# Kernel optimization log

Measured on AMD Instinct MI355X. Metric: run time of the kernel, lower is better.

Reference implementation:

```python
import jax, jax.numpy as jnp
import numpy as np

DIM = 2048
NHEAD = 16
HEAD_DIM = DIM // NHEAD
FF_HIDDEN = 5632
EPS = 1e-6


def setup_inputs() -> dict:
    key = jax.random.key(0)
    ks = jax.random.split(key, 8)
    B, S = 2, 2048
    sd = 0.02
    return {
        "x": jax.random.normal(ks[0], (B, S, DIM), dtype=jnp.float32),
        "w_qkv": jax.random.normal(ks[1], (DIM, 3 * DIM), dtype=jnp.float32) * sd,
        "w_out": jax.random.normal(ks[2], (DIM, DIM), dtype=jnp.float32) * sd,
        "g1": jnp.ones((DIM,), dtype=jnp.float32),
        "g2": jnp.ones((DIM,), dtype=jnp.float32),
        "w1": jax.random.normal(ks[3], (DIM, FF_HIDDEN), dtype=jnp.float32) * sd,
        "w3": jax.random.normal(ks[4], (DIM, FF_HIDDEN), dtype=jnp.float32) * sd,
        "w2": jax.random.normal(ks[5], (FF_HIDDEN, DIM), dtype=jnp.float32) * sd,
    }


def _rmsnorm(x, g):
    rms = jnp.sqrt(jnp.mean(x * x, axis=-1, keepdims=True) + EPS)
    return x / rms * g


def _attention(x, w_qkv, w_out):
    B, S, D = x.shape
    qkv = x @ w_qkv  # [B,S,3D]
    q, k, v = jnp.split(qkv, 3, axis=-1)
    # [B,H,S,hd]
    q = q.reshape(B, S, NHEAD, HEAD_DIM).transpose(0, 2, 1, 3)
    k = k.reshape(B, S, NHEAD, HEAD_DIM).transpose(0, 2, 1, 3)
    v = v.reshape(B, S, NHEAD, HEAD_DIM).transpose(0, 2, 1, 3)
    scores = jnp.einsum("bhqd,bhkd->bhqk", q, k) / jnp.sqrt(jnp.float32(HEAD_DIM))
    causal = jnp.tril(jnp.ones((S, S), dtype=bool))
    scores = jnp.where(causal, scores, -jnp.inf)
    attn = jax.nn.softmax(scores, axis=-1)
    out = jnp.einsum("bhqk,bhkd->bhqd", attn, v)
    out = out.transpose(0, 2, 1, 3).reshape(B, S, D)
    return out @ w_out


def _swiglu(x, w1, w3, w2):
    return (jax.nn.silu(x @ w1) * (x @ w3)) @ w2


def reference(x, w_qkv, w_out, g1, g2, w1, w3, w2):
    x = x + _attention(_rmsnorm(x, g1), w_qkv, w_out)
    x = x + _swiglu(_rmsnorm(x, g2), w1, w3, w2)
    return x
```

## Files before the change

### kernel.cpp

```cpp
#include <hip/hip_runtime.h>
#include <hip/hip_bf16.h>
#include <stdint.h>


typedef __attribute__((ext_vector_type(8))) short bf16x8;
typedef __attribute__((ext_vector_type(8))) unsigned short u16x8;
typedef __attribute__((ext_vector_type(4))) float f32x4;

__device__ __forceinline__ unsigned short f2bf(float f) {
  union { float f; unsigned int u; } c; c.f = f;
  unsigned int u = c.u + 0x7fffu + ((c.u >> 16) & 1u);
  return (unsigned short)(u >> 16);
}
__device__ __forceinline__ float bf2f(unsigned short h) {
  union { unsigned int u; float f; } c; c.u = ((unsigned int)h) << 16;
  return c.f;
}

__device__ __forceinline__ void gload16(const void* g, void* l) {
  __builtin_amdgcn_global_load_lds(
      (const __attribute__((address_space(1))) void*)g,
      (__attribute__((address_space(3))) void*)l, 16, 0, 0);
}

__global__ __launch_bounds__(256)
void rmsnorm_bf16(const float* __restrict__ x, const float* __restrict__ g,
                  unsigned short* __restrict__ y)
{
  const long row = blockIdx.x;
  const float* xr = x + row * 2048;
  const int t = threadIdx.x;
  float4 a = *(const float4*)(xr + t * 8);
  float4 b = *(const float4*)(xr + t * 8 + 4);
  float ss = a.x*a.x + a.y*a.y + a.z*a.z + a.w*a.w
           + b.x*b.x + b.y*b.y + b.z*b.z + b.w*b.w;
#pragma unroll
  for (int off = 32; off >= 1; off >>= 1) ss += __shfl_xor(ss, off, 64);
  __shared__ float sm[4];
  if ((t & 63) == 0) sm[t >> 6] = ss;
  __syncthreads();
  float inv = rsqrtf((sm[0] + sm[1] + sm[2] + sm[3]) * (1.0f / 2048.0f) + 1e-6f);
  float4 ga = *(const float4*)(g + t * 8);
  float4 gb = *(const float4*)(g + t * 8 + 4);
  u16x8 ov;
  ov[0] = f2bf(a.x * inv * ga.x); ov[1] = f2bf(a.y * inv * ga.y);
  ov[2] = f2bf(a.z * inv * ga.z); ov[3] = f2bf(a.w * inv * ga.w);
  ov[4] = f2bf(b.x * inv * gb.x); ov[5] = f2bf(b.y * inv * gb.y);
  ov[6] = f2bf(b.z * inv * gb.z); ov[7] = f2bf(b.w * inv * gb.w);
  *(u16x8*)(y + row * 2048 + t * 8) = ov;
}

__global__ __launch_bounds__(256)
void transpose_w(const float* __restrict__ in, unsigned short* __restrict__ outp,
                 int K, int N)
{
  __shared__ float tile[32][33];
  const int c0 = blockIdx.x * 32, r0 = blockIdx.y * 32;
  const int cx = threadIdx.x & 31, ry = threadIdx.x >> 5;
#pragma unroll
  for (int i = 0; i < 4; i++)
    tile[ry + i * 8][cx] = in[(long)(r0 + ry + i * 8) * N + c0 + cx];
  __syncthreads();
#pragma unroll
  for (int i = 0; i < 4; i++)
    outp[(long)(c0 + ry + i * 8) * K + r0 + cx] = f2bf(tile[cx][ry + i * 8]);
}

template<int EPI>
__global__ __launch_bounds__(256)
void gemm_bt(const unsigned short* __restrict__ A,
             const unsigned short* __restrict__ Bt,
             void* __restrict__ Cout,
             const float* __restrict__ res,
             const unsigned short* __restrict__ mulsrc,
             int M, int N, int K)
{
  __shared__ unsigned short lds[2 * 128 * 64];
  const int tid = threadIdx.x;
  const int lane = tid & 63, wave = tid >> 6;
  const int wr = wave >> 1, wc = wave & 1;
  const int l15 = lane & 15, lg = lane >> 4;
  const long m0 = (long)blockIdx.y * 128, n0 = (long)blockIdx.x * 128;

  f32x4 acc[4][4];
#pragma unroll
  for (int m = 0; m < 4; m++)
#pragma unroll
    for (int n = 0; n < 4; n++) acc[m][n] = f32x4{0.f, 0.f, 0.f, 0.f};

  const int rsub = lane >> 3;
  const int csw  = (lane & 7) ^ rsub;
  const unsigned short* Ab = A  + (m0 + wave * 32 + rsub) * (long)K + csw * 8;
  const unsigned short* Bb = Bt + (n0 + wave * 32 + rsub) * (long)K + csw * 8;
  unsigned short* Al = lds + wave * 2048;
  unsigned short* Bl = lds + 8192 + wave * 2048;

  for (int kt = 0; kt < K; kt += 64) {
    __syncthreads();
#pragma unroll
    for (int i = 0; i < 4; i++) {
      gload16(Ab + (long)(i * 8) * K + kt, Al + i * 512);
      gload16(Bb + (long)(i * 8) * K + kt, Bl + i * 512);
    }
    __syncthreads();
#pragma unroll
    for (int kc = 0; kc < 2; kc++) {
      bf16x8 af[4], bfr[4];
#pragma unroll
      for (int m = 0; m < 4; m++) {
        int row = wr * 64 + m * 16 + l15;
        int off = row * 128 + ((kc * 64 + lg * 16) ^ ((row & 7) << 4));
        af[m] = *(const bf16x8*)((const char*)lds + off);
      }
#pragma unroll
      for (int n = 0; n < 4; n++) {
        int row = wc * 64 + n * 16 + l15;
        int off = 16384 + row * 128 + ((kc * 64 + lg * 16) ^ ((row & 7) << 4));
        bfr[n] = *(const bf16x8*)((const char*)lds + off);
      }
#pragma unroll
      for (int m = 0; m < 4; m++)
#pragma unroll
        for (int n = 0; n < 4; n++)
          acc[m][n] = __builtin_amdgcn_mfma_f32_16x16x32_bf16(af[m], bfr[n], acc[m][n], 0, 0, 0);
    }
  }

  if (EPI == 3) {
#pragma unroll
    for (int m = 0; m < 4; m++)
#pragma unroll
      for (int n = 0; n < 4; n++)
#pragma unroll
        for (int r = 0; r < 4; r++) {
          long row = m0 + wr * 64 + m * 16 + lg * 4 + r;
          long col = n0 + wc * 64 + n * 16 + l15;
          ((float*)Cout)[row * N + col] = acc[m][n][r] + res[row * N + col];
        }
    return;
  }

  __syncthreads();
  unsigned short* Cl = lds;
#pragma unroll
  for (int m = 0; m < 4; m++)
#pragma unroll
    for (int n = 0; n < 4; n++)
#pragma unroll
      for (int r = 0; r < 4; r++) {
        float v = acc[m][n][r];
        if (EPI == 1) v = v / (1.f + __expf(-v));
        Cl[(wr * 64 + m * 16 + lg * 4 + r) * 128 + wc * 64 + n * 16 + l15] = f2bf(v);
      }
  __syncthreads();
#pragma unroll
  for (int r8 = 0; r8 < 8; r8++) {
    int id = tid + r8 * 256;
    int row = id >> 4, c = (id & 15) * 8;
    long grow = m0 + row, gcol = n0 + c;
    u16x8 v = *(const u16x8*)(Cl + row * 128 + c);
    if (EPI == 2) {
      u16x8 mm = *(const u16x8*)(mulsrc + grow * N + gcol);
#pragma unroll
      for (int j = 0; j < 8; j++) v[j] = f2bf(bf2f(v[j]) * bf2f(mm[j]));
    }
    *(u16x8*)((unsigned short*)Cout + grow * N + gcol) = v;
  }
}

__global__ __launch_bounds__(256)
void attn_fwd(const unsigned short* __restrict__ qkv, unsigned short* __restrict__ out)
{
  __shared__ unsigned short Klds[64 * 128];
  __shared__ unsigned short Vt[128 * 64];
  __shared__ unsigned short Plds[4][16 * 64];
  const int tid = threadIdx.x, lane = tid & 63, w = tid >> 6;
  const int l15 = lane & 15, lg = lane >> 4;
  const int qb = blockIdx.x * 64;
  const int b = blockIdx.y >> 4, hh = blockIdx.y & 15;
  const long rstride = 6144;
  const long base = (long)b * 2048 * 6144;
  const int qoff = hh * 128, koff = 2048 + hh * 128, voff = 4096 + hh * 128;

  bf16x8 qf[4];
  {
    long qrow = qb + w * 16 + l15;
#pragma unroll
    for (int kc = 0; kc < 4; kc++)
      qf[kc] = *(const bf16x8*)(qkv + base + qrow * rstride + qoff + kc * 32 + lg * 8);
  }
  f32x4 o[8];
#pragma unroll
  for (int dg = 0; dg < 8; dg++) o[dg] = f32x4{0.f, 0.f, 0.f, 0.f};
  float mrow[4] = {-1e30f, -1e30f, -1e30f, -1e30f};
  float lrow[4] = {0.f, 0.f, 0.f, 0.f};
  const float scale = 0.08838834764831845f;

  const int s_st = tid >> 4;
  const int d0 = (tid & 15) * 8;

  const int nt = blockIdx.x + 1;
  for (int t = 0; t < nt; t++) {
    const long kvb = base + (long)(t * 64) * rstride;
#pragma unroll
    for (int i = 0; i < 4; i++) {
      int srow = s_st + i * 16;
      uint4 kk = *(const uint4*)(qkv + kvb + (long)srow * rstride + koff + d0);
      *(uint4*)((char*)Klds + ((srow * 256 + d0 * 2) ^ ((srow & 7) << 4))) = kk;
      u16x8 vv = *(const u16x8*)(qkv + kvb + (long)srow * rstride + voff + d0);
#pragma unroll
      for (int j = 0; j < 8; j++) {
        int d = d0 + j;
        int xr = (((d >> 3) ^ d) & 7) << 4;
        *((unsigned short*)((char*)Vt + ((d * 128 + srow * 2) ^ xr))) = vv[j];
      }
    }
    __syncthreads();

    f32x4 sacc[4];
#pragma unroll
    for (int cg = 0; cg < 4; cg++) {
      f32x4 a = f32x4{0.f, 0.f, 0.f, 0.f};
#pragma unroll
      for (int kc = 0; kc < 4; kc++) {
        int krow = cg * 16 + l15;
        bf16x8 kf = *(const bf16x8*)((char*)Klds +
                      ((krow * 256 + kc * 64 + lg * 16) ^ ((krow & 7) << 4)));
        a = __builtin_amdgcn_mfma_f32_16x16x32_bf16(qf[kc], kf, a, 0, 0, 0);
      }
      sacc[cg] = a;
    }

    float p[4][4];
    float pm[4];
    const bool diag = (t == nt - 1);
#pragma unroll
    for (int r = 0; r < 4; r++) pm[r] = -1e30f;
#pragma unroll
    for (int cg = 0; cg < 4; cg++)
#pragma unroll
      for (int r = 0; r < 4; r++) {
        float v = sacc[cg][r] * scale;
        if (diag) {
          int kvg = t * 64 + cg * 16 + l15;
          int qg = qb + w * 16 + lg * 4 + r;
          if (kvg > qg) v = -1e30f;
        }
        p[cg][r] = v;
        pm[r] = fmaxf(pm[r], v);
      }
#pragma unroll
    for (int r = 0; r < 4; r++) {
#pragma unroll
      for (int off = 1; off < 16; off <<= 1)
        pm[r] = fmaxf(pm[r], __shfl_xor(pm[r], off, 64));
      float mn = fmaxf(mrow[r], pm[r]);
      float al = __expf(mrow[r] - mn);
      mrow[r] = mn;
      float s = 0.f;
#pragma unroll
      for (int cg = 0; cg < 4; cg++) { p[cg][r] = __expf(p[cg][r] - mn); s += p[cg][r]; }
#pragma unroll
      for (int off = 1; off < 16; off <<= 1)
        s += __shfl_xor(s, off, 64);
      lrow[r] = lrow[r] * al + s;
#pragma unroll
      for (int dg = 0; dg < 8; dg++) o[dg][r] *= al;
    }

#pragma unroll
    for (int cg = 0; cg < 4; cg++)
#pragma unroll
      for (int r = 0; r < 4; r++) {
        int q = lg * 4 + r;
        *((unsigned short*)((char*)&Plds[w][0] +
            ((q * 128 + (cg * 16 + l15) * 2) ^ ((q & 7) << 4)))) = f2bf(p[cg][r]);
      }
    asm volatile("s_waitcnt lgkmcnt(0)" ::: "memory");
    __builtin_amdgcn_sched_barrier(0);

#pragma unroll
    for (int kc = 0; kc < 2; kc++) {
      bf16x8 pa = *(const bf16x8*)((char*)&Plds[w][0] +
                    ((l15 * 128 + kc * 64 + lg * 16) ^ ((l15 & 7) << 4)));
#pragma unroll
      for (int dg = 0; dg < 8; dg++) {
        int d = dg * 16 + l15;
        int xr = (((d >> 3) ^ d) & 7) << 4;
        bf16x8 vf = *(const bf16x8*)((char*)Vt + ((d * 128 + kc * 64 + lg * 16) ^ xr));
        o[dg] = __builtin_amdgcn_mfma_f32_16x16x32_bf16(pa, vf, o[dg], 0, 0, 0);
      }
    }
    __syncthreads();
  }

#pragma unroll
  for (int r = 0; r < 4; r++) {
    float inv = 1.f / lrow[r];
    long row = (long)b * 2048 + qb + w * 16 + lg * 4 + r;
#pragma unroll
    for (int dg = 0; dg < 8; dg++)
      out[row * 2048 + hh * 128 + dg * 16 + l15] = f2bf(o[dg][r] * inv);
  }
}

extern "C" void kernel_launch(void* const* d_in, const int* in_sizes, int n_in,
                              void* d_out, int out_size, void* d_ws, size_t ws_size,
                              hipStream_t stream)
{
  const float* x     = (const float*)d_in[0];
  const float* w_qkv = (const float*)d_in[1];
  const float* w_out = (const float*)d_in[2];
  const float* g1    = (const float*)d_in[3];
  const float* g2    = (const float*)d_in[4];
  const float* w1    = (const float*)d_in[5];
  const float* w3    = (const float*)d_in[6];
  const float* w2    = (const float*)d_in[7];
  float* outp = (float*)d_out;
  char* ws = (char*)d_ws;

  unsigned short* wT  = (unsigned short*)(ws);
  unsigned short* y   = (unsigned short*)(ws + 25165824);
  unsigned short* qkv = (unsigned short*)(ws + 41943040);
  unsigned short* att = (unsigned short*)(ws + 92274688);
  float*          x1  = (float*)(ws + 109051904);
  unsigned short* s1  = (unsigned short*)(ws + 142606336);
  unsigned short* h   = qkv;

  rmsnorm_bf16<<<4096, 256, 0, stream>>>(x, g1, y);
  transpose_w<<<dim3(6144 / 32, 2048 / 32), 256, 0, stream>>>(w_qkv, wT, 2048, 6144);
  gemm_bt<0><<<dim3(48, 32), 256, 0, stream>>>(y, wT, qkv, nullptr, nullptr, 4096, 6144, 2048);
  attn_fwd<<<dim3(32, 32), 256, 0, stream>>>(qkv, att);
  transpose_w<<<dim3(64, 64), 256, 0, stream>>>(w_out, wT, 2048, 2048);
  gemm_bt<3><<<dim3(16, 32), 256, 0, stream>>>(att, wT, x1, x, nullptr, 4096, 2048, 2048);

  rmsnorm_bf16<<<4096, 256, 0, stream>>>(x1, g2, y);
  transpose_w<<<dim3(176, 64), 256, 0, stream>>>(w1, wT, 2048, 5632);
  gemm_bt<1><<<dim3(44, 32), 256, 0, stream>>>(y, wT, s1, nullptr, nullptr, 4096, 5632, 2048);
  transpose_w<<<dim3(176, 64), 256, 0, stream>>>(w3, wT, 2048, 5632);
  gemm_bt<2><<<dim3(44, 32), 256, 0, stream>>>(y, wT, h, nullptr, s1, 4096, 5632, 2048);
  transpose_w<<<dim3(64, 176), 256, 0, stream>>>(w2, wT, 5632, 2048);
  gemm_bt<3><<<dim3(16, 32), 256, 0, stream>>>(h, wT, outp, x1, nullptr, 4096, 2048, 5632);
}
```

Baseline: 791.9 us.

## Pair causal attention query blocks, pre-transpose V, and remap GEMM workgroups

Attention now gives each workgroup a pair of query blocks (ip and 31-ip), so every workgroup does the same amount of causal work and shares each K/V tile load between both blocks. A separate transpose_v kernel writes V transposed into scratch so the attention kernel can fill LDS with vector stores instead of scalar scattered ones. The kernel also adds s_setprio around the MFMA sections and launch_bounds(256,2), and the GEMM gets an XCD-style workgroup index remap meant to improve L2 locality. The costs are an extra kernel launch plus V round-tripping through memory, and higher register pressure from holding two query states.

```diff
diff --git a/kernel.cpp b/kernel.cpp
--- a/kernel.cpp
+++ b/kernel.cpp
@@ -66,6 +66,24 @@
     outp[(long)(c0 + ry + i * 8) * K + r0 + cx] = f2bf(tile[cx][ry + i * 8]);
 }
 
+__global__ __launch_bounds__(256)
+void transpose_v(const unsigned short* __restrict__ qkv, unsigned short* __restrict__ vT)
+{
+  __shared__ unsigned short tile[32][34];
+  const int bh = blockIdx.z, b = bh >> 4, hh = bh & 15;
+  const int s0 = blockIdx.x * 32, d0 = blockIdx.y * 32;
+  const int cx = threadIdx.x & 31, ry = threadIdx.x >> 5;
+  const unsigned short* src = qkv + (long)b * 2048 * 6144 + 4096 + hh * 128;
+#pragma unroll
+  for (int i = 0; i < 4; i++)
+    tile[ry + i * 8][cx] = src[(long)(s0 + ry + i * 8) * 6144 + d0 + cx];
+  __syncthreads();
+  unsigned short* o = vT + ((long)bh * 128 + d0) * 2048 + s0;
+#pragma unroll
+  for (int i = 0; i < 4; i++)
+    o[(long)(ry + i * 8) * 2048 + cx] = tile[cx][ry + i * 8];
+}
+
 template<int EPI>
 __global__ __launch_bounds__(256)
 void gemm_bt(const unsigned short* __restrict__ A,
@@ -80,7 +98,12 @@
   const int lane = tid & 63, wave = tid >> 6;
   const int wr = wave >> 1, wc = wave & 1;
   const int l15 = lane & 15, lg = lane >> 4;
-  const long m0 = (long)blockIdx.y * 128, n0 = (long)blockIdx.x * 128;
+
+  const int nwg = gridDim.x * gridDim.y;
+  int wg = blockIdx.y * gridDim.x + blockIdx.x;
+  wg = (wg & 7) * (nwg >> 3) + (wg >> 3);
+  const int bx = wg % gridDim.x, by = wg / gridDim.x;
+  const long m0 = (long)by * 128, n0 = (long)bx * 128;
 
   f32x4 acc[4][4];
 #pragma unroll
@@ -168,139 +191,160 @@
   }
 }
 
-__global__ __launch_bounds__(256)
-void attn_fwd(const unsigned short* __restrict__ qkv, unsigned short* __restrict__ out)
+#define QSTEP(qf, mrow, lrow, o, qb, isdiag) do {                              \
+    f32x4 sacc[4];                                                             \
+    __builtin_amdgcn_s_setprio(1);                                             \
+    _Pragma("unroll")                                                          \
+    for (int cg = 0; cg < 4; cg++) {                                           \
+      f32x4 a = f32x4{0.f, 0.f, 0.f, 0.f};                                     \
+      _Pragma("unroll")                                                        \
+      for (int kc = 0; kc < 4; kc++) {                                         \
+        int krow = cg * 16 + l15;                                              \
+        bf16x8 kf = *(const bf16x8*)((char*)Klds +                             \
+            (krow * 256 + ((kc * 64 + lg * 16) ^ ((krow & 7) << 4))));         \
+        a = __builtin_amdgcn_mfma_f32_16x16x32_bf16(qf[kc], kf, a, 0, 0, 0);   \
+      }                                                                        \
+      sacc[cg] = a;                                                            \
+    }                                                                          \
+    __builtin_amdgcn_s_setprio(0);                                             \
+    float p[4][4], pm[4];                                                      \
+    _Pragma("unroll")                                                          \
+    for (int r = 0; r < 4; r++) pm[r] = -1e30f;                                \
+    _Pragma("unroll")                                                          \
+    for (int cg = 0; cg < 4; cg++)                                             \
+      _Pragma("unroll")                                                        \
+      for (int r = 0; r < 4; r++) {                                            \
+        float v = sacc[cg][r] * scale;                                         \
+        if (isdiag) {                                                          \
+          int kvg = kv0 + cg * 16 + l15;                                       \
+          int qg = qb + w * 16 + lg * 4 + r;                                   \
+          if (kvg > qg) v = -1e30f;                                            \
+        }                                                                      \
+        p[cg][r] = v;                                                          \
+        pm[r] = fmaxf(pm[r], v);                                               \
+      }                                                                        \
+    _Pragma("unroll")                                                          \
+    for (int r = 0; r < 4; r++) {                                              \
+      _Pragma("unroll")                                                        \
+      for (int off = 1; off < 16; off <<= 1)                                   \
+        pm[r] = fmaxf(pm[r], __shfl_xor(pm[r], off, 64));                      \
+      float mn = fmaxf(mrow[r], pm[r]);                                        \
+      float al = __expf(mrow[r] - mn);                                         \
+      mrow[r] = mn;                                                            \
+      float s = 0.f;                                                           \
+      _Pragma("unroll")                                                        \
+      for (int cg = 0; cg < 4; cg++) { p[cg][r] = __expf(p[cg][r] - mn); s += p[cg][r]; } \
+      _Pragma("unroll")                                                        \
+      for (int off = 1; off < 16; off <<= 1)                                   \
+        s += __shfl_xor(s, off, 64);                                           \
+      lrow[r] = lrow[r] * al + s;                                              \
+      _Pragma("unroll")                                                        \
+      for (int dg = 0; dg < 8; dg++) o[dg][r] *= al;                           \
+    }                                                                          \
+    _Pragma("unroll")                                                          \
+    for (int cg = 0; cg < 4; cg++)                                             \
+      _Pragma("unroll")                                                        \
+      for (int r = 0; r < 4; r++) {                                            \
+        int q = lg * 4 + r;                                                    \
+        *((unsigned short*)((char*)&Plds[w][0] +                               \
+            (q * 128 + (((cg * 16 + l15) * 2) ^ ((q & 7) << 4))))) = f2bf(p[cg][r]); \
+      }                                                                        \
+    asm volatile("s_waitcnt lgkmcnt(0)" ::: "memory");                         \
+    __builtin_amdgcn_sched_barrier(0);                                         \
+    __builtin_amdgcn_s_setprio(1);                                             \
+    _Pragma("unroll")                                                          \
+    for (int kc = 0; kc < 2; kc++) {                                           \
+      bf16x8 pa = *(const bf16x8*)((char*)&Plds[w][0] +                        \
+          (l15 * 128 + ((kc * 64 + lg * 16) ^ ((l15 & 7) << 4))));             \
+      _Pragma("unroll")                                                        \
+      for (int dg = 0; dg < 8; dg++) {                                         \
+        int d = dg * 16 + l15;                                                 \
+        bf16x8 vf = *(const bf16x8*)((char*)Vlds +                             \
+            (d * 128 + ((kc * 64 + lg * 16) ^ ((d & 7) << 4))));               \
+        o[dg] = __builtin_amdgcn_mfma_f32_16x16x32_bf16(pa, vf, o[dg], 0, 0, 0); \
+      }                                                                        \
+    }                                                                          \
+    __builtin_amdgcn_s_setprio(0);                                             \
+  } while (0)
+
+__global__ __launch_bounds__(256, 2)
+void attn_fwd(const unsigned short* __restrict__ qkv,
+              const unsigned short* __restrict__ vT,
+              unsigned short* __restrict__ out)
 {
   __shared__ unsigned short Klds[64 * 128];
-  __shared__ unsigned short Vt[128 * 64];
+  __shared__ unsigned short Vlds[128 * 64];
   __shared__ unsigned short Plds[4][16 * 64];
   const int tid = threadIdx.x, lane = tid & 63, w = tid >> 6;
   const int l15 = lane & 15, lg = lane >> 4;
-  const int qb = blockIdx.x * 64;
-  const int b = blockIdx.y >> 4, hh = blockIdx.y & 15;
-  const long rstride = 6144;
+
+  const int nwg = gridDim.x * gridDim.y;
+  int wg = blockIdx.y * gridDim.x + blockIdx.x;
+  wg = (wg & 7) * (nwg >> 3) + (wg >> 3);
+  const int ip = wg % 16;
+  const int bh = wg / 16;
+  const int b = bh >> 4, hh = bh & 15;
+
+  const int qbA = ip * 64, qbB = (31 - ip) * 64;
   const long base = (long)b * 2048 * 6144;
-  const int qoff = hh * 128, koff = 2048 + hh * 128, voff = 4096 + hh * 128;
-
-  bf16x8 qf[4];
+  const int qoff = hh * 128, koff = 2048 + hh * 128;
+  const unsigned short* vTg = vT + (long)bh * (128 * 2048);
+
+  bf16x8 qfA[4], qfB[4];
   {
-    long qrow = qb + w * 16 + l15;
-#pragma unroll
-    for (int kc = 0; kc < 4; kc++)
-      qf[kc] = *(const bf16x8*)(qkv + base + qrow * rstride + qoff + kc * 32 + lg * 8);
-  }
-  f32x4 o[8];
-#pragma unroll
-  for (int dg = 0; dg < 8; dg++) o[dg] = f32x4{0.f, 0.f, 0.f, 0.f};
-  float mrow[4] = {-1e30f, -1e30f, -1e30f, -1e30f};
-  float lrow[4] = {0.f, 0.f, 0.f, 0.f};
+    long qrA = qbA + w * 16 + l15, qrB = qbB + w * 16 + l15;
+#pragma unroll
+    for (int kc = 0; kc < 4; kc++) {
+      qfA[kc] = *(const bf16x8*)(qkv + base + qrA * 6144 + qoff + kc * 32 + lg * 8);
+      qfB[kc] = *(const bf16x8*)(qkv + base + qrB * 6144 + qoff + kc * 32 + lg * 8);
+    }
+  }
+  f32x4 oA[8], oB[8];
+#pragma unroll
+  for (int dg = 0; dg < 8; dg++) {
+    oA[dg] = f32x4{0.f, 0.f, 0.f, 0.f};
+    oB[dg] = f32x4{0.f, 0.f, 0.f, 0.f};
+  }
+  float mA[4] = {-1e30f, -1e30f, -1e30f, -1e30f}, lA[4] = {0.f, 0.f, 0.f, 0.f};
+  float mB[4] = {-1e30f, -1e30f, -1e30f, -1e30f}, lB[4] = {0.f, 0.f, 0.f, 0.f};
   const float scale = 0.08838834764831845f;
 
-  const int s_st = tid >> 4;
-  const int d0 = (tid & 15) * 8;
-
-  const int nt = blockIdx.x + 1;
+  const int s_st = tid >> 4, d0 = (tid & 15) * 8;
+  const int vrow = tid >> 3, vc = tid & 7;
+
+  const int nt = 32 - ip;
   for (int t = 0; t < nt; t++) {
-    const long kvb = base + (long)(t * 64) * rstride;
-#pragma unroll
-    for (int i = 0; i < 4; i++) {
-      int srow = s_st + i * 16;
-      uint4 kk = *(const uint4*)(qkv + kvb + (long)srow * rstride + koff + d0);
-      *(uint4*)((char*)Klds + ((srow * 256 + d0 * 2) ^ ((srow & 7) << 4))) = kk;
-      u16x8 vv = *(const u16x8*)(qkv + kvb + (long)srow * rstride + voff + d0);
-#pragma unroll
-      for (int j = 0; j < 8; j++) {
-        int d = d0 + j;
-        int xr = (((d >> 3) ^ d) & 7) << 4;
-        *((unsigned short*)((char*)Vt + ((d * 128 + srow * 2) ^ xr))) = vv[j];
-      }
+    const int kv0 = t * 64;
+#pragma unroll
+    for (int u = 0; u < 4; u++) {
+      int srow = s_st + u * 16;
+      uint4 kk = *(const uint4*)(qkv + base + (long)(kv0 + srow) * 6144 + koff + d0);
+      *(uint4*)((char*)Klds + (srow * 256 + ((d0 * 2) ^ ((srow & 7) << 4)))) = kk;
+    }
+#pragma unroll
+    for (int u = 0; u < 4; u++) {
+      int d = vrow + u * 32;
+      uint4 vv = *(const uint4*)(vTg + (long)d * 2048 + kv0 + vc * 8);
+      *(uint4*)((char*)Vlds + (d * 128 + ((vc * 16) ^ ((d & 7) << 4)))) = vv;
     }
     __syncthreads();
 
-    f32x4 sacc[4];
-#pragma unroll
-    for (int cg = 0; cg < 4; cg++) {
-      f32x4 a = f32x4{0.f, 0.f, 0.f, 0.f};
-#pragma unroll
-      for (int kc = 0; kc < 4; kc++) {
-        int krow = cg * 16 + l15;
-        bf16x8 kf = *(const bf16x8*)((char*)Klds +
-                      ((krow * 256 + kc * 64 + lg * 16) ^ ((krow & 7) << 4)));
-        a = __builtin_amdgcn_mfma_f32_16x16x32_bf16(qf[kc], kf, a, 0, 0, 0);
-      }
-      sacc[cg] = a;
-    }
-
-    float p[4][4];
-    float pm[4];
-    const bool diag = (t == nt - 1);
-#pragma unroll
-    for (int r = 0; r < 4; r++) pm[r] = -1e30f;
-#pragma unroll
-    for (int cg = 0; cg < 4; cg++)
-#pragma unroll
-      for (int r = 0; r < 4; r++) {
-        float v = sacc[cg][r] * scale;
-        if (diag) {
-          int kvg = t * 64 + cg * 16 + l15;
-          int qg = qb + w * 16 + lg * 4 + r;
-          if (kvg > qg) v = -1e30f;
-        }
-        p[cg][r] = v;
-        pm[r] = fmaxf(pm[r], v);
-      }
-#pragma unroll
-    for (int r = 0; r < 4; r++) {
-#pragma unroll
-      for (int off = 1; off < 16; off <<= 1)
-        pm[r] = fmaxf(pm[r], __shfl_xor(pm[r], off, 64));
-      float mn = fmaxf(mrow[r], pm[r]);
-      float al = __expf(mrow[r] - mn);
-      mrow[r] = mn;
-      float s = 0.f;
-#pragma unroll
-      for (int cg = 0; cg < 4; cg++) { p[cg][r] = __expf(p[cg][r] - mn); s += p[cg][r]; }
-#pragma unroll
-      for (int off = 1; off < 16; off <<= 1)
-        s += __shfl_xor(s, off, 64);
-      lrow[r] = lrow[r] * al + s;
-#pragma unroll
-      for (int dg = 0; dg < 8; dg++) o[dg][r] *= al;
-    }
-
-#pragma unroll
-    for (int cg = 0; cg < 4; cg++)
-#pragma unroll
-      for (int r = 0; r < 4; r++) {
-        int q = lg * 4 + r;
-        *((unsigned short*)((char*)&Plds[w][0] +
-            ((q * 128 + (cg * 16 + l15) * 2) ^ ((q & 7) << 4)))) = f2bf(p[cg][r]);
-      }
-    asm volatile("s_waitcnt lgkmcnt(0)" ::: "memory");
-    __builtin_amdgcn_sched_barrier(0);
-
-#pragma unroll
-    for (int kc = 0; kc < 2; kc++) {
-      bf16x8 pa = *(const bf16x8*)((char*)&Plds[w][0] +
-                    ((l15 * 128 + kc * 64 + lg * 16) ^ ((l15 & 7) << 4)));
-#pragma unroll
-      for (int dg = 0; dg < 8; dg++) {
-        int d = dg * 16 + l15;
-        int xr = (((d >> 3) ^ d) & 7) << 4;
-        bf16x8 vf = *(const bf16x8*)((char*)Vt + ((d * 128 + kc * 64 + lg * 16) ^ xr));
-        o[dg] = __builtin_amdgcn_mfma_f32_16x16x32_bf16(pa, vf, o[dg], 0, 0, 0);
-      }
-    }
+    if (t <= ip) QSTEP(qfA, mA, lA, oA, qbA, (t == ip));
+    QSTEP(qfB, mB, lB, oB, qbB, (t == nt - 1));
+
     __syncthreads();
   }
 
 #pragma unroll
   for (int r = 0; r < 4; r++) {
-    float inv = 1.f / lrow[r];
-    long row = (long)b * 2048 + qb + w * 16 + lg * 4 + r;
-#pragma unroll
-    for (int dg = 0; dg < 8; dg++)
-      out[row * 2048 + hh * 128 + dg * 16 + l15] = f2bf(o[dg][r] * inv);
+    float invA = 1.f / lA[r], invB = 1.f / lB[r];
+    long rowA = (long)b * 2048 + qbA + w * 16 + lg * 4 + r;
+    long rowB = (long)b * 2048 + qbB + w * 16 + lg * 4 + r;
+#pragma unroll
+    for (int dg = 0; dg < 8; dg++) {
+      out[rowA * 2048 + hh * 128 + dg * 16 + l15] = f2bf(oA[dg][r] * invA);
+      out[rowB * 2048 + hh * 128 + dg * 16 + l15] = f2bf(oB[dg][r] * invB);
+    }
   }
 }
 
@@ -325,12 +369,14 @@
   unsigned short* att = (unsigned short*)(ws + 92274688);
   float*          x1  = (float*)(ws + 109051904);
   unsigned short* s1  = (unsigned short*)(ws + 142606336);
+  unsigned short* vTb = s1;
   unsigned short* h   = qkv;
 
   rmsnorm_bf16<<<4096, 256, 0, stream>>>(x, g1, y);
   transpose_w<<<dim3(6144 / 32, 2048 / 32), 256, 0, stream>>>(w_qkv, wT, 2048, 6144);
   gemm_bt<0><<<dim3(48, 32), 256, 0, stream>>>(y, wT, qkv, nullptr, nullptr, 4096, 6144, 2048);
-  attn_fwd<<<dim3(32, 32), 256, 0, stream>>>(qkv, att);
+  transpose_v<<<dim3(64, 4, 32), 256, 0, stream>>>(qkv, vTb);
+  attn_fwd<<<dim3(16, 32), 256, 0, stream>>>(qkv, vTb, att);
   transpose_w<<<dim3(64, 64), 256, 0, stream>>>(w_out, wT, 2048, 2048);
   gemm_bt<3><<<dim3(16, 32), 256, 0, stream>>>(att, wT, x1, x, nullptr, 4096, 2048, 2048);
 
```

After: 716.5 us. 9.5% less time.
